# Kernel optimization log

Hardware: AMD Instinct MI355X
Metric: run time of the kernel (lower is better)

The kernel has to match this reference:

```python
import jax, jax.numpy as jnp
import numpy as np
import math

D = 32
H = 4
DH = D // H
N_LAYERS = 2
SEQ_LEN = 6
VOCAB = 15
B = 131072


def setup_inputs() -> dict:
    key = jax.random.key(0)
    ks = jax.random.split(key, 9)
    return {
        "tokens": jax.random.randint(ks[0], (B, SEQ_LEN), 0, VOCAB),
        "tok_emb": jax.random.normal(ks[1], (VOCAB, D), jnp.float32) * 0.1,
        "pos_emb": jax.random.normal(ks[2], (SEQ_LEN, D), jnp.float32) * 0.1,
        "Wq": jax.random.normal(ks[3], (N_LAYERS, D, D), jnp.float32) * 0.1,
        "Wk": jax.random.normal(ks[4], (N_LAYERS, D, D), jnp.float32) * 0.1,
        "Wv": jax.random.normal(ks[5], (N_LAYERS, D, D), jnp.float32) * 0.1,
        "Wo": jax.random.normal(ks[6], (N_LAYERS, D, D), jnp.float32) * 0.1,
        "W1": jax.random.normal(ks[7], (N_LAYERS, D, 4 * D), jnp.float32) * 0.1,
        "W2": jax.random.normal(ks[8], (N_LAYERS, 4 * D, D), jnp.float32) * 0.1,
    }


def _layer_norm(x, eps=1e-5):
    mu = jnp.mean(x, axis=-1, keepdims=True)
    var = jnp.var(x, axis=-1, keepdims=True)
    return (x - mu) * jax.lax.rsqrt(var + eps)


def reference(tokens, tok_emb, pos_emb, Wq, Wk, Wv, Wo, W1, W2):
    Bb, S = tokens.shape
    X = tok_emb[tokens] + pos_emb[:S]  # [B,S,D]
    causal_mask = jnp.triu(jnp.full((S, S), -jnp.inf, jnp.float32), k=1)
    scale = 1.0 / math.sqrt(DH)
    for L in range(N_LAYERS):
        Xn = _layer_norm(X)
        Q = jnp.einsum('bsd,de->bse', Xn, Wq[L]).reshape(Bb, S, H, DH)
        K = jnp.einsum('bsd,de->bse', Xn, Wk[L]).reshape(Bb, S, H, DH)
        V = jnp.einsum('bsd,de->bse', Xn, Wv[L]).reshape(Bb, S, H, DH)
        scores = jnp.einsum('bshk,bthk->bhst', Q, K) * scale + causal_mask
        A = jax.nn.softmax(scores, axis=-1)
        O = jnp.einsum('bhst,bthk->bshk', A, V).reshape(Bb, S, D)
        X = X + jnp.einsum('bsd,de->bse', O, Wo[L])
        Xn = _layer_norm(X)
        HID = jax.nn.gelu(jnp.einsum('bsd,de->bse', Xn, W1[L]), approximate=False)
        X = X + jnp.einsum('bse,ed->bsd', HID, W2[L])
    X = _layer_norm(X)
    logits = jnp.einsum('bsd,vd->bsv', X, tok_emb)
    return logits
```

## Files before the change

### kernel.cpp

```cpp
#include <hip/hip_runtime.h>

#define SEQ 6
#define THREADS 256
#define ELB 40
#define NL 2
#define VOC 15

typedef __attribute__((ext_vector_type(8))) _Float16 h8;
typedef __attribute__((ext_vector_type(2))) _Float16 h2;
typedef __attribute__((ext_vector_type(4))) float    f32x4;

#define XN 0
#define KP 4096
#define SMEM_U32 8192


__device__ __forceinline__ unsigned int pkh(float a, float b) {
    auto h = __builtin_amdgcn_cvt_pkrtz(a, b);
    return __builtin_bit_cast(unsigned int, h);
}
__device__ __forceinline__ h8 ldh(const unsigned int* p) {
    uint4 u = *(const uint4*)p;
    return __builtin_bit_cast(h8, u);
}
#if __has_builtin(__builtin_amdgcn_fdot2)
__device__ __forceinline__ float dot2acc(unsigned int a, unsigned int b, float c) {
    return __builtin_amdgcn_fdot2(__builtin_bit_cast(h2, a), __builtin_bit_cast(h2, b), c, false);
}
__device__ __forceinline__ float dot2h(h2 a, h2 b, float c) {
    return __builtin_amdgcn_fdot2(a, b, c, false);
}
#else
__device__ __forceinline__ float dot2acc(unsigned int a, unsigned int b, float c) {
    h2 ha = __builtin_bit_cast(h2, a), hb = __builtin_bit_cast(h2, b);
    return fmaf((float)ha.y, (float)hb.y, fmaf((float)ha.x, (float)hb.x, c));
}
__device__ __forceinline__ float dot2h(h2 a, h2 b, float c) {
    return fmaf((float)a.y, (float)b.y, fmaf((float)a.x, (float)b.x, c));
}
#endif
#define H2C(v) ((h2){(_Float16)(v), (_Float16)(v)})
__device__ __forceinline__ unsigned int gelu2(float a, float b) {
    h2 xp = __builtin_bit_cast(h2, pkh(a, b));
#if __has_builtin(__builtin_elementwise_max) && __has_builtin(__builtin_elementwise_min)
    h2 xc = __builtin_elementwise_min(__builtin_elementwise_max(xp, H2C(-3.0f)), H2C(3.0f));
#else
    h2 xc = __builtin_bit_cast(h2, pkh(fminf(fmaxf(a, -3.0f), 3.0f),
                                       fminf(fmaxf(b, -3.0f), 3.0f)));
#endif
    h2 u = xc * xc;
    h2 p = H2C(4.80757e-5f);
    p = p * u + H2C(-1.40632e-3f);
    p = p * u + H2C(1.75795e-2f);
    p = p * u + H2C(-1.30947e-1f);
    p = p * u + H2C(7.9714e-1f);
    h2 hx = xp * H2C(0.5f);
    h2 r  = (hx * xc) * p + hx;
    return __builtin_bit_cast(unsigned int, r);
}
__device__ __forceinline__ int permc(int p) {
    int h = (p & 15) >> 2, j = p & 3, hi = p >> 4;
    return 8*h + 2*j + hi;
}
__device__ __forceinline__ int swg(int row, int g) {
    return ((g ^ ((row >> 1) & 3)) << 2);
}
__device__ __forceinline__ void ln_write(const h2* X2, unsigned int* base, int row) {
    const h2 one = H2C(1.0f);
    float mu = 0.f;
    #pragma unroll
    for (int w = 0; w < 16; ++w) mu = dot2h(X2[w], one, mu);
    mu *= 0.03125f;
    h2 mu2 = __builtin_bit_cast(h2, pkh(mu, mu));
    float var = 0.f;
    #pragma unroll
    for (int w = 0; w < 16; ++w) { h2 d = X2[w] - mu2; var = dot2h(d, d, var); }
    var *= 0.03125f;
    float rs = rsqrtf(var + 1e-5f), b = -mu * rs;
    h2 rs2 = __builtin_bit_cast(h2, pkh(rs, rs));
    h2 b2  = __builtin_bit_cast(h2, pkh(b, b));
    unsigned int* rp = base + row * 16;
    const int k = (row >> 1) & 3;
    #pragma unroll
    for (int g = 0; g < 4; ++g) {
        uint4 w;
        w.x = __builtin_bit_cast(unsigned int, X2[4*g+0] * rs2 + b2);
        w.y = __builtin_bit_cast(unsigned int, X2[4*g+1] * rs2 + b2);
        w.z = __builtin_bit_cast(unsigned int, X2[4*g+2] * rs2 + b2);
        w.w = __builtin_bit_cast(unsigned int, X2[4*g+3] * rs2 + b2);
        *(uint4*)&rp[(g ^ k) << 2] = w;
    }
}

__global__ __launch_bounds__(64) void prep(
    const float* __restrict__ temb, const float* __restrict__ wq,
    const float* __restrict__ wk, const float* __restrict__ wv,
    const float* __restrict__ wo, const float* __restrict__ w1,
    const float* __restrict__ w2, unsigned int* __restrict__ ws)
{
    const int part = blockIdx.x;
    const int t = threadIdx.x;
    if (part == 24) {
        for (int i = t; i < 256; i += 64) {
            int c = i >> 4, w = i & 15;
            ws[12288 + i] = (c < VOC) ? pkh(temb[c*32 + w], temb[c*32 + w + 16]) : 0u;
        }
        return;
    }
    const int L = part / 12, m = part % 12;
    unsigned int* o = ws + L * 6144;
    for (int i = t; i < 512; i += 64) {
        int c = i >> 4, w = i & 15;
        if (m < 3) {
            const float* M = (m == 0 ? wq : (m == 1 ? wk : wv)) + L*1024;
            int pc = permc(c);
            o[m*512 + i] = pkh(M[w*32 + pc], M[(w+16)*32 + pc]);
        } else if (m == 3) {
            const float* M = wo + L*1024;
            o[1536 + i] = pkh(M[permc(w)*32 + c], M[permc(w+16)*32 + c]);
        } else if (m < 8) {
            int q = m - 4;
            const float* M = w1 + L*4096;
            o[2048 + q*1024 + i] = pkh(M[w*128 + 32*q + c], M[(w+16)*128 + 32*q + c]);
        } else {
            int q = m - 8;
            const float* M = w2 + L*4096;
            o[2048 + q*1024 + 512 + i] = pkh(M[(32*q+w)*32 + c], M[(32*q+16+w)*32 + c]);
        }
    }
}

__global__ __launch_bounds__(THREADS, 3)
void tf_mfma(const int* __restrict__ toks, const float* __restrict__ temb,
             const float* __restrict__ pemb, const unsigned int* __restrict__ ws,
             float* __restrict__ out, int nelem)
{
    __shared__ unsigned int S[SMEM_U32];
    const int tid  = threadIdx.x;
    const int lane = tid & 63;
    const int wid  = tid >> 6;
    const int llo  = lane & 15, lhi = lane >> 4;
    const int boff = 4 * lhi;
    int le = lane / 6;
    int s  = lane - le * 6;
    if (le > 9) { le = 9; s = 5; }
    const int rb   = wid*64 + le*6;
    const int myk  = (tid >> 1) & 3;
    const int elem = blockIdx.x * ELB + wid*10 + le;
    const f32x4 zz = {0.f, 0.f, 0.f, 0.f};

    h2 X2[16];
    {
        const int ti  = (elem < nelem) ? (elem*SEQ + s) : 0;
        const int tok = toks[ti];
        #pragma unroll
        for (int g = 0; g < 4; ++g) {
            float4 alo = *(const float4*)&temb[tok*32 + 4*g];
            float4 ahi = *(const float4*)&temb[tok*32 + 16 + 4*g];
            float4 plo = *(const float4*)&pemb[s*32 + 4*g];
            float4 phi = *(const float4*)&pemb[s*32 + 16 + 4*g];
            X2[4*g+0] = __builtin_bit_cast(h2, pkh(alo.x + plo.x, ahi.x + phi.x));
            X2[4*g+1] = __builtin_bit_cast(h2, pkh(alo.y + plo.y, ahi.y + phi.y));
            X2[4*g+2] = __builtin_bit_cast(h2, pkh(alo.z + plo.z, ahi.z + phi.z));
            X2[4*g+3] = __builtin_bit_cast(h2, pkh(alo.w + plo.w, ahi.w + phi.w));
        }
    }

    #pragma unroll 1
    for (int L = 0; L < NL; ++L) {
        const unsigned int* wsL = ws + L * 6144;

        ln_write(X2, &S[XN], tid);

        uint4 q4[4];
        {
            h8 bq0 = ldh(wsL +          llo    *16 + boff);
            h8 bq1 = ldh(wsL +         (llo+16)*16 + boff);
            h8 bk0 = ldh(wsL +  512 +   llo    *16 + boff);
            h8 bk1 = ldh(wsL +  512 +  (llo+16)*16 + boff);
            h8 bv0 = ldh(wsL + 1024 +   llo    *16 + boff);
            h8 bv1 = ldh(wsL + 1024 +  (llo+16)*16 + boff);
            h8 aa[4];
            #pragma unroll
            for (int j = 0; j < 4; ++j) {
                int rowa = wid*64 + j*16 + llo;
                aa[j] = ldh(&S[XN + rowa*16 + swg(rowa, lhi)]);
            }
            #pragma unroll
            for (int j = 0; j < 4; ++j) {
                f32x4 k0 = __builtin_amdgcn_mfma_f32_16x16x32_f16(aa[j], bk0, zz, 0,0,0);
                f32x4 k1 = __builtin_amdgcn_mfma_f32_16x16x32_f16(aa[j], bk1, zz, 0,0,0);
                int rowb = wid*64 + j*16 + lhi*4;
                #pragma unroll
                for (int rg = 0; rg < 4; ++rg) {
                    int row = rowb + rg;
                    S[KP + row*16 + swg(row, llo >> 2) + (llo & 3)] = pkh(k0[rg], k1[rg]);
                }
            }
            #pragma unroll
            for (int j = 0; j < 4; ++j) {
                f32x4 qa = __builtin_amdgcn_mfma_f32_16x16x32_f16(aa[j], bq0, zz, 0,0,0);
                f32x4 qb = __builtin_amdgcn_mfma_f32_16x16x32_f16(aa[j], bq1, zz, 0,0,0);
                int rowb = wid*64 + j*16 + lhi*4;
                #pragma unroll
                for (int rg = 0; rg < 4; ++rg) {
                    int row = rowb + rg;
                    S[XN + row*16 + swg(row, llo >> 2) + (llo & 3)] = pkh(qa[rg], qb[rg]);
                }
            }
            #pragma unroll
            for (int h = 0; h < 4; ++h)
                q4[h] = *(const uint4*)&S[XN + tid*16 + ((h ^ myk) << 2)];
            #pragma unroll
            for (int j = 0; j < 4; ++j) {
                f32x4 v0 = __builtin_amdgcn_mfma_f32_16x16x32_f16(aa[j], bv0, zz, 0,0,0);
                f32x4 v1 = __builtin_amdgcn_mfma_f32_16x16x32_f16(aa[j], bv1, zz, 0,0,0);
                int rowb = wid*64 + j*16 + lhi*4;
                #pragma unroll
                for (int rg = 0; rg < 4; ++rg) {
                    int row = rowb + rg;
                    S[XN + row*16 + swg(row, llo >> 2) + (llo & 3)] = pkh(v0[rg], v1[rg]);
                }
            }
        }

        {
            float den[4] = {0.f, 0.f, 0.f, 0.f};
            h2 O[16];
            #pragma unroll
            for (int w = 0; w < 16; ++w) O[w] = __builtin_bit_cast(h2, 0u);
            #pragma unroll
            for (int t = 0; t < SEQ; ++t) {
                int krow = rb + t;
                const unsigned int* kr = &S[KP + krow*16];
                const unsigned int* vr = &S[XN + krow*16];
                int kk4 = (krow >> 1) & 3;
                float msk = (t <= s) ? 0.f : -1e30f;
                #pragma unroll
                for (int h = 0; h < 4; ++h) {
                    uint4 kk = *(const uint4*)&kr[(h ^ kk4) << 2];
                    float d = dot2acc(q4[h].x, kk.x, 0.f);
                    d = dot2acc(q4[h].y, kk.y, d);
                    d = dot2acc(q4[h].z, kk.z, d);
                    d = dot2acc(q4[h].w, kk.w, d);
                    float e = exp2f(fmaf(d, 0.51006975f, msk));
                    den[h] += e;
                    h2 wg2 = __builtin_bit_cast(h2, pkh(e, e));
                    uint4 vv = *(const uint4*)&vr[(h ^ kk4) << 2];
                    O[4*h+0] += __builtin_bit_cast(h2, vv.x) * wg2;
                    O[4*h+1] += __builtin_bit_cast(h2, vv.y) * wg2;
                    O[4*h+2] += __builtin_bit_cast(h2, vv.z) * wg2;
                    O[4*h+3] += __builtin_bit_cast(h2, vv.w) * wg2;
                }
            }
            #pragma unroll
            for (int h = 0; h < 4; ++h) {
                float rdh = __builtin_amdgcn_rcpf(den[h]);
                h2 rr = __builtin_bit_cast(h2, pkh(rdh, rdh));
                O[4*h+0] *= rr; O[4*h+1] *= rr; O[4*h+2] *= rr; O[4*h+3] *= rr;
            }
            #pragma unroll
            for (int g = 0; g < 4; ++g) {
                uint4 w;
                w.x = __builtin_bit_cast(unsigned int, O[4*g+0]);
                w.y = __builtin_bit_cast(unsigned int, O[4*g+1]);
                w.z = __builtin_bit_cast(unsigned int, O[4*g+2]);
                w.w = __builtin_bit_cast(unsigned int, O[4*g+3]);
                *(uint4*)&S[KP + tid*16 + ((g ^ myk) << 2)] = w;
            }
        }

        {
            h8 bo0 = ldh(wsL + 1536 +  llo    *16 + boff);
            h8 bo1 = ldh(wsL + 1536 + (llo+16)*16 + boff);
            #pragma unroll
            for (int j = 0; j < 4; ++j) {
                int rowa = wid*64 + j*16 + llo;
                h8 a = ldh(&S[KP + rowa*16 + swg(rowa, lhi)]);
                f32x4 o0 = __builtin_amdgcn_mfma_f32_16x16x32_f16(a, bo0, zz, 0,0,0);
                f32x4 o1 = __builtin_amdgcn_mfma_f32_16x16x32_f16(a, bo1, zz, 0,0,0);
                int rowb = wid*64 + j*16 + lhi*4;
                #pragma unroll
                for (int rg = 0; rg < 4; ++rg) {
                    int row = rowb + rg;
                    S[XN + row*16 + swg(row, llo >> 2) + (llo & 3)] = pkh(o0[rg], o1[rg]);
                }
            }
        }
        #pragma unroll
        for (int g = 0; g < 4; ++g) {
            uint4 v = *(const uint4*)&S[XN + tid*16 + ((g ^ myk) << 2)];
            X2[4*g+0] += __builtin_bit_cast(h2, v.x);
            X2[4*g+1] += __builtin_bit_cast(h2, v.y);
            X2[4*g+2] += __builtin_bit_cast(h2, v.z);
            X2[4*g+3] += __builtin_bit_cast(h2, v.w);
        }
        ln_write(X2, &S[KP], tid);

        f32x4 cf[4][2];
        #pragma unroll
        for (int j = 0; j < 4; ++j) { cf[j][0] = zz; cf[j][1] = zz; }
        #pragma unroll
        for (int q = 0; q < 4; ++q) {
            const unsigned int* wq4 = wsL + 2048 + q*1024;
            h8 b10 = ldh(wq4 +        llo    *16 + boff);
            h8 b11 = ldh(wq4 +       (llo+16)*16 + boff);
            h8 b20 = ldh(wq4 + 512 +  llo    *16 + boff);
            h8 b21 = ldh(wq4 + 512 + (llo+16)*16 + boff);
            #pragma unroll
            for (int j = 0; j < 4; ++j) {
                int rowa = wid*64 + j*16 + llo;
                h8 a = ldh(&S[KP + rowa*16 + swg(rowa, lhi)]);
                f32x4 h0 = __builtin_amdgcn_mfma_f32_16x16x32_f16(a, b10, zz, 0,0,0);
                f32x4 h1 = __builtin_amdgcn_mfma_f32_16x16x32_f16(a, b11, zz, 0,0,0);
                int rowb = wid*64 + j*16 + lhi*4;
                #pragma unroll
                for (int rg = 0; rg < 4; ++rg) {
                    int row = rowb + rg;
                    S[XN + row*16 + swg(row, llo >> 2) + (llo & 3)] = gelu2(h0[rg], h1[rg]);
                }
            }
            #pragma unroll
            for (int j = 0; j < 4; ++j) {
                int rowa = wid*64 + j*16 + llo;
                h8 ah = ldh(&S[XN + rowa*16 + swg(rowa, lhi)]);
                cf[j][0] = __builtin_amdgcn_mfma_f32_16x16x32_f16(ah, b20, cf[j][0], 0,0,0);
                cf[j][1] = __builtin_amdgcn_mfma_f32_16x16x32_f16(ah, b21, cf[j][1], 0,0,0);
            }
        }
        #pragma unroll
        for (int j = 0; j < 4; ++j) {
            int rowb = wid*64 + j*16 + lhi*4;
            #pragma unroll
            for (int rg = 0; rg < 4; ++rg) {
                int row = rowb + rg;
                S[XN + row*16 + swg(row, llo >> 2) + (llo & 3)] = pkh(cf[j][0][rg], cf[j][1][rg]);
            }
        }
        #pragma unroll
        for (int g = 0; g < 4; ++g) {
            uint4 v = *(const uint4*)&S[XN + tid*16 + ((g ^ myk) << 2)];
            X2[4*g+0] += __builtin_bit_cast(h2, v.x);
            X2[4*g+1] += __builtin_bit_cast(h2, v.y);
            X2[4*g+2] += __builtin_bit_cast(h2, v.z);
            X2[4*g+3] += __builtin_bit_cast(h2, v.w);
        }
    }

    ln_write(X2, &S[XN], tid);
    {
        h8 bt = ldh(ws + 12288 + llo*16 + boff);
        #pragma unroll
        for (int j = 0; j < 4; ++j) {
            int rowa = wid*64 + j*16 + llo;
            h8 a = ldh(&S[XN + rowa*16 + swg(rowa, lhi)]);
            f32x4 lg = __builtin_amdgcn_mfma_f32_16x16x32_f16(a, bt, zz, 0,0,0);
            int rowb = wid*64 + j*16 + lhi*4;
            #pragma unroll
            for (int rg = 0; rg < 4; ++rg) {
                int row = rowb + rg;
                S[KP + row*16 + swg(row, llo >> 2) + (llo & 3)] = __float_as_uint(lg[rg]);
            }
        }
    }
    __syncthreads();
    {
        const long long obase = (long long)blockIdx.x * (ELB*SEQ*VOC);
        const long long tot   = (long long)nelem * (SEQ*VOC);
        for (int i = tid; i < ELB*SEQ*VOC; i += THREADS) {
            if (obase + i < tot) {
                int rl   = i / VOC, col = i - rl*VOC;
                int w    = rl / 60, r6 = rl - w*60;
                int slot = w*64 + r6;
                out[obase + i] = __uint_as_float(
                    S[KP + slot*16 + (((col >> 2) ^ ((slot >> 1) & 3)) << 2) + (col & 3)]);
            }
        }
    }
}

extern "C" void kernel_launch(void* const* d_in, const int* in_sizes, int n_in,
                              void* d_out, int out_size, void* d_ws, size_t ws_size,
                              hipStream_t stream) {
    const int*   toks = (const int*)  d_in[0];
    const float* temb = (const float*)d_in[1];
    const float* pemb = (const float*)d_in[2];
    const float* wq   = (const float*)d_in[3];
    const float* wk   = (const float*)d_in[4];
    const float* wv   = (const float*)d_in[5];
    const float* wo   = (const float*)d_in[6];
    const float* w1   = (const float*)d_in[7];
    const float* w2   = (const float*)d_in[8];
    unsigned int* ws  = (unsigned int*)d_ws;
    float* out = (float*)d_out;
    const int nelem = in_sizes[0] / SEQ;
    const int nblk  = (nelem + ELB - 1) / ELB;

    prep<<<dim3(25), dim3(64), 0, stream>>>(temb, wq, wk, wv, wo, w1, w2, ws);
    tf_mfma<<<dim3(nblk), dim3(THREADS), 0, stream>>>(toks, temb, pemb, ws, out, nelem);
}
```

Before: 141.8 us.

## Swap MFMA operands so outputs are stored as 128-bit LDS writes

Swaps the A and B operands of every MFMA so each lane produces four consecutive columns of one row (a transposed output). This lets the results be packed into a single uint4 LDS store at the same swizzled offset used for the A-operand loads, replacing four scalar stores. The per-lane row offsets are precomputed once, and the layer-norm output for the FFN is loaded into registers once instead of per q-chunk. Correctness depends on the transposed output layout matching the swizzle pattern the later vector reads expect.

```diff
diff --git a/kernel.cpp b/kernel.cpp
--- a/kernel.cpp
+++ b/kernel.cpp
@@ -149,6 +149,13 @@
     const int elem = blockIdx.x * ELB + wid*10 + le;
     const f32x4 zz = {0.f, 0.f, 0.f, 0.f};
 
+    int tOff[4];
+    #pragma unroll
+    for (int j = 0; j < 4; ++j) {
+        int rowa = wid*64 + j*16 + llo;
+        tOff[j] = rowa*16 + swg(rowa, lhi);
+    }
+
     h2 X2[16];
     {
         const int ti  = (elem < nelem) ? (elem*SEQ + s) : 0;
@@ -182,45 +189,36 @@
             h8 bv1 = ldh(wsL + 1024 +  (llo+16)*16 + boff);
             h8 aa[4];
             #pragma unroll
-            for (int j = 0; j < 4; ++j) {
-                int rowa = wid*64 + j*16 + llo;
-                aa[j] = ldh(&S[XN + rowa*16 + swg(rowa, lhi)]);
-            }
-            #pragma unroll
-            for (int j = 0; j < 4; ++j) {
-                f32x4 k0 = __builtin_amdgcn_mfma_f32_16x16x32_f16(aa[j], bk0, zz, 0,0,0);
-                f32x4 k1 = __builtin_amdgcn_mfma_f32_16x16x32_f16(aa[j], bk1, zz, 0,0,0);
-                int rowb = wid*64 + j*16 + lhi*4;
-                #pragma unroll
-                for (int rg = 0; rg < 4; ++rg) {
-                    int row = rowb + rg;
-                    S[KP + row*16 + swg(row, llo >> 2) + (llo & 3)] = pkh(k0[rg], k1[rg]);
-                }
-            }
-            #pragma unroll
-            for (int j = 0; j < 4; ++j) {
-                f32x4 qa = __builtin_amdgcn_mfma_f32_16x16x32_f16(aa[j], bq0, zz, 0,0,0);
-                f32x4 qb = __builtin_amdgcn_mfma_f32_16x16x32_f16(aa[j], bq1, zz, 0,0,0);
-                int rowb = wid*64 + j*16 + lhi*4;
-                #pragma unroll
-                for (int rg = 0; rg < 4; ++rg) {
-                    int row = rowb + rg;
-                    S[XN + row*16 + swg(row, llo >> 2) + (llo & 3)] = pkh(qa[rg], qb[rg]);
-                }
+            for (int j = 0; j < 4; ++j) aa[j] = ldh(&S[XN + tOff[j]]);
+            #pragma unroll
+            for (int j = 0; j < 4; ++j) {
+                f32x4 k0 = __builtin_amdgcn_mfma_f32_16x16x32_f16(bk0, aa[j], zz, 0,0,0);
+                f32x4 k1 = __builtin_amdgcn_mfma_f32_16x16x32_f16(bk1, aa[j], zz, 0,0,0);
+                uint4 w;
+                w.x = pkh(k0[0], k1[0]); w.y = pkh(k0[1], k1[1]);
+                w.z = pkh(k0[2], k1[2]); w.w = pkh(k0[3], k1[3]);
+                *(uint4*)&S[KP + tOff[j]] = w;
+            }
+            #pragma unroll
+            for (int j = 0; j < 4; ++j) {
+                f32x4 qa = __builtin_amdgcn_mfma_f32_16x16x32_f16(bq0, aa[j], zz, 0,0,0);
+                f32x4 qb = __builtin_amdgcn_mfma_f32_16x16x32_f16(bq1, aa[j], zz, 0,0,0);
+                uint4 w;
+                w.x = pkh(qa[0], qb[0]); w.y = pkh(qa[1], qb[1]);
+                w.z = pkh(qa[2], qb[2]); w.w = pkh(qa[3], qb[3]);
+                *(uint4*)&S[XN + tOff[j]] = w;
             }
             #pragma unroll
             for (int h = 0; h < 4; ++h)
                 q4[h] = *(const uint4*)&S[XN + tid*16 + ((h ^ myk) << 2)];
             #pragma unroll
             for (int j = 0; j < 4; ++j) {
-                f32x4 v0 = __builtin_amdgcn_mfma_f32_16x16x32_f16(aa[j], bv0, zz, 0,0,0);
-                f32x4 v1 = __builtin_amdgcn_mfma_f32_16x16x32_f16(aa[j], bv1, zz, 0,0,0);
-                int rowb = wid*64 + j*16 + lhi*4;
-                #pragma unroll
-                for (int rg = 0; rg < 4; ++rg) {
-                    int row = rowb + rg;
-                    S[XN + row*16 + swg(row, llo >> 2) + (llo & 3)] = pkh(v0[rg], v1[rg]);
-                }
+                f32x4 v0 = __builtin_amdgcn_mfma_f32_16x16x32_f16(bv0, aa[j], zz, 0,0,0);
+                f32x4 v1 = __builtin_amdgcn_mfma_f32_16x16x32_f16(bv1, aa[j], zz, 0,0,0);
+                uint4 w;
+                w.x = pkh(v0[0], v1[0]); w.y = pkh(v0[1], v1[1]);
+                w.z = pkh(v0[2], v1[2]); w.w = pkh(v0[3], v1[3]);
+                *(uint4*)&S[XN + tOff[j]] = w;
             }
         }
 
@@ -275,16 +273,13 @@
             h8 bo1 = ldh(wsL + 1536 + (llo+16)*16 + boff);
             #pragma unroll
             for (int j = 0; j < 4; ++j) {
-                int rowa = wid*64 + j*16 + llo;
-                h8 a = ldh(&S[KP + rowa*16 + swg(rowa, lhi)]);
-                f32x4 o0 = __builtin_amdgcn_mfma_f32_16x16x32_f16(a, bo0, zz, 0,0,0);
-                f32x4 o1 = __builtin_amdgcn_mfma_f32_16x16x32_f16(a, bo1, zz, 0,0,0);
-                int rowb = wid*64 + j*16 + lhi*4;
-                #pragma unroll
-                for (int rg = 0; rg < 4; ++rg) {
-                    int row = rowb + rg;
-                    S[XN + row*16 + swg(row, llo >> 2) + (llo & 3)] = pkh(o0[rg], o1[rg]);
-                }
+                h8 a = ldh(&S[KP + tOff[j]]);
+                f32x4 o0 = __builtin_amdgcn_mfma_f32_16x16x32_f16(bo0, a, zz, 0,0,0);
+                f32x4 o1 = __builtin_amdgcn_mfma_f32_16x16x32_f16(bo1, a, zz, 0,0,0);
+                uint4 w;
+                w.x = pkh(o0[0], o1[0]); w.y = pkh(o0[1], o1[1]);
+                w.z = pkh(o0[2], o1[2]); w.w = pkh(o0[3], o1[3]);
+                *(uint4*)&S[XN + tOff[j]] = w;
             }
         }
         #pragma unroll
@@ -297,6 +292,9 @@
         }
         ln_write(X2, &S[KP], tid);
 
+        h8 aa2[4];
+        #pragma unroll
+        for (int j = 0; j < 4; ++j) aa2[j] = ldh(&S[KP + tOff[j]]);
         f32x4 cf[4][2];
         #pragma unroll
         for (int j = 0; j < 4; ++j) { cf[j][0] = zz; cf[j][1] = zz; }
@@ -309,33 +307,26 @@
             h8 b21 = ldh(wq4 + 512 + (llo+16)*16 + boff);
             #pragma unroll
             for (int j = 0; j < 4; ++j) {
-                int rowa = wid*64 + j*16 + llo;
-                h8 a = ldh(&S[KP + rowa*16 + swg(rowa, lhi)]);
-                f32x4 h0 = __builtin_amdgcn_mfma_f32_16x16x32_f16(a, b10, zz, 0,0,0);
-                f32x4 h1 = __builtin_amdgcn_mfma_f32_16x16x32_f16(a, b11, zz, 0,0,0);
-                int rowb = wid*64 + j*16 + lhi*4;
-                #pragma unroll
-                for (int rg = 0; rg < 4; ++rg) {
-                    int row = rowb + rg;
-                    S[XN + row*16 + swg(row, llo >> 2) + (llo & 3)] = gelu2(h0[rg], h1[rg]);
-                }
-            }
-            #pragma unroll
-            for (int j = 0; j < 4; ++j) {
-                int rowa = wid*64 + j*16 + llo;
-                h8 ah = ldh(&S[XN + rowa*16 + swg(rowa, lhi)]);
-                cf[j][0] = __builtin_amdgcn_mfma_f32_16x16x32_f16(ah, b20, cf[j][0], 0,0,0);
-                cf[j][1] = __builtin_amdgcn_mfma_f32_16x16x32_f16(ah, b21, cf[j][1], 0,0,0);
+                f32x4 h0 = __builtin_amdgcn_mfma_f32_16x16x32_f16(b10, aa2[j], zz, 0,0,0);
+                f32x4 h1 = __builtin_amdgcn_mfma_f32_16x16x32_f16(b11, aa2[j], zz, 0,0,0);
+                uint4 w;
+                w.x = gelu2(h0[0], h1[0]); w.y = gelu2(h0[1], h1[1]);
+                w.z = gelu2(h0[2], h1[2]); w.w = gelu2(h0[3], h1[3]);
+                *(uint4*)&S[XN + tOff[j]] = w;
+            }
+            #pragma unroll
+            for (int j = 0; j < 4; ++j) {
+                h8 ah = ldh(&S[XN + tOff[j]]);
+                cf[j][0] = __builtin_amdgcn_mfma_f32_16x16x32_f16(b20, ah, cf[j][0], 0,0,0);
+                cf[j][1] = __builtin_amdgcn_mfma_f32_16x16x32_f16(b21, ah, cf[j][1], 0,0,0);
             }
         }
         #pragma unroll
         for (int j = 0; j < 4; ++j) {
-            int rowb = wid*64 + j*16 + lhi*4;
-            #pragma unroll
-            for (int rg = 0; rg < 4; ++rg) {
-                int row = rowb + rg;
-                S[XN + row*16 + swg(row, llo >> 2) + (llo & 3)] = pkh(cf[j][0][rg], cf[j][1][rg]);
-            }
+            uint4 w;
+            w.x = pkh(cf[j][0][0], cf[j][1][0]); w.y = pkh(cf[j][0][1], cf[j][1][1]);
+            w.z = pkh(cf[j][0][2], cf[j][1][2]); w.w = pkh(cf[j][0][3], cf[j][1][3]);
+            *(uint4*)&S[XN + tOff[j]] = w;
         }
         #pragma unroll
         for (int g = 0; g < 4; ++g) {
@@ -352,15 +343,12 @@
         h8 bt = ldh(ws + 12288 + llo*16 + boff);
         #pragma unroll
         for (int j = 0; j < 4; ++j) {
-            int rowa = wid*64 + j*16 + llo;
-            h8 a = ldh(&S[XN + rowa*16 + swg(rowa, lhi)]);
-            f32x4 lg = __builtin_amdgcn_mfma_f32_16x16x32_f16(a, bt, zz, 0,0,0);
-            int rowb = wid*64 + j*16 + lhi*4;
-            #pragma unroll
-            for (int rg = 0; rg < 4; ++rg) {
-                int row = rowb + rg;
-                S[KP + row*16 + swg(row, llo >> 2) + (llo & 3)] = __float_as_uint(lg[rg]);
-            }
+            h8 a = ldh(&S[XN + tOff[j]]);
+            f32x4 lg = __builtin_amdgcn_mfma_f32_16x16x32_f16(bt, a, zz, 0,0,0);
+            uint4 w;
+            w.x = __float_as_uint(lg[0]); w.y = __float_as_uint(lg[1]);
+            w.z = __float_as_uint(lg[2]); w.w = __float_as_uint(lg[3]);
+            *(uint4*)&S[KP + tOff[j]] = w;
         }
     }
     __syncthreads();
```

Result: faster. 132.6 us (-6.5%).
